# Kernel optimization log

Hardware: AMD Instinct MI355X
Metric: run time of the kernel (lower is better)

The kernel has to match this reference:

```python
import jax, jax.numpy as jnp
import numpy as np

D_HEAD = 64

def setup_inputs() -> dict:
    key = jax.random.key(0)
    kq, kk, kv, kc = jax.random.split(key, 4)
    B, H, T, D = 2, 16, 2048, D_HEAD
    Q = jax.random.normal(kq, (B, H, T, D), dtype=jnp.float32)
    K = jax.random.normal(kk, (B, H, T, D), dtype=jnp.float32)
    V = jax.random.normal(kv, (B, H, T, D), dtype=jnp.float32)
    # causal mask: True = attend
    mask = jnp.tril(jnp.ones((T, T), dtype=jnp.bool_))
    curvature = jax.random.normal(kc, (H, D, D), dtype=jnp.float32) * 0.02
    return {"Q": Q, "K": K, "V": V, "mask": mask, "curvature": curvature}

def reference(Q, K, V, mask, curvature):
    scale = 1.0 / np.sqrt(Q.shape[-1]).astype(np.float32)
    # per-head learned rotation of Q
    Q_rot = jnp.einsum('bhtd,hde->bhte', Q, curvature)
    scores = jnp.einsum('bhtd,bhsd->bhts', Q_rot, K) * scale  # [B,H,T,T]
    scores = jnp.where(mask[None, None, :, :], scores, -jnp.inf)
    attn = jax.nn.softmax(scores, axis=-1)
    out = jnp.einsum('bhts,bhsd->bhtd', attn, V)
    return out
```

## Files before the change

kernel.cpp:

```cpp
#include <hip/hip_runtime.h>


typedef __attribute__((ext_vector_type(8))) short short8;
typedef __attribute__((ext_vector_type(8))) unsigned short ushort8;
typedef __attribute__((ext_vector_type(4))) float f32x4;
typedef __attribute__((ext_vector_type(2))) _Float16 half2v;
typedef __attribute__((ext_vector_type(4))) _Float16 half4;
typedef __attribute__((ext_vector_type(8))) _Float16 half8;

constexpr int Tc = 2048;
constexpr int Dc = 64;
constexpr size_t REGION = (size_t)32 * Tc * Dc;

__device__ inline unsigned short f2bf(float f) {
    union { float f; unsigned u; } x; x.f = f;
    return (unsigned short)((x.u + 0x7fffu + ((x.u >> 16) & 1u)) >> 16);
}

__device__ inline half2v pkrtz(float a, float b) {
    return __builtin_bit_cast(half2v, __builtin_amdgcn_cvt_pkrtz(a, b));
}

#define MFMA_BF16_K32(a, b, c) __builtin_amdgcn_mfma_f32_16x16x32_bf16((a), (b), (c), 0, 0, 0)
#define MFMA_F16_K16(a, b, c)  __builtin_amdgcn_mfma_f32_16x16x16f16((a), (b), (c), 0, 0, 0)

__global__ __launch_bounds__(256, 1)
void holo_cfrag(const float* __restrict__ Cp, unsigned short* __restrict__ cfrag_g)
{
    const int t = threadIdx.x, lane = t & 63, eb = t >> 6;
    const int l15 = lane & 15, quad = lane >> 4;
    const int h = blockIdx.x;
    const float* Cg = Cp + (size_t)h * Dc * Dc;
    #pragma unroll
    for (int half = 0; half < 2; ++half) {
        short8 b;
        #pragma unroll
        for (int jj = 0; jj < 8; ++jj) {
            const int d = half * 32 + quad * 8 + jj;
            b[jj] = (short)f2bf(Cg[d * Dc + eb * 16 + l15]);
        }
        *(short8*)(&cfrag_g[(((size_t)h * 4 + eb) * 2 + half) * 512 + lane * 8]) = b;
    }
}

__global__ __launch_bounds__(256, 4)
void holo_prep8(const float* __restrict__ Qp, const float* __restrict__ Kp,
                const float* __restrict__ Vp,
                const unsigned short* __restrict__ cfrag_g,
                unsigned short* __restrict__ qfrag_g,
                unsigned short* __restrict__ kfrag_g,
                _Float16* __restrict__ vfrag_g)
{
    __shared__ unsigned short kt[64 * 72];
    __shared__ unsigned short qt[64 * 72];
    __shared__ _Float16      vt[64 * 72];
    __shared__ unsigned short pf[64 * 72];

    const int t = threadIdx.x, lane = t & 63, w = t >> 6;
    const int l15 = lane & 15, quad = lane >> 4, wb = w * 16;
    const int n = blockIdx.x, bh = n >> 5, st = n & 31, h = bh & 15;
    const int s0 = st * 64;

    const float* Qg = Qp + ((size_t)bh * Tc + s0) * Dc;
    const float* Kg = Kp + ((size_t)bh * Tc + s0) * Dc;
    const float* Vg = Vp + ((size_t)bh * Tc + s0) * Dc;

    #pragma unroll
    for (int kk = 0; kk < 4; ++kk) {
        const int flat = kk * 1024 + t * 4;
        const int r = flat >> 6, d0 = flat & 63;
        float4 kv = *(const float4*)(&Kg[flat]);
        ushort4 kp; kp.x = f2bf(kv.x); kp.y = f2bf(kv.y); kp.z = f2bf(kv.z); kp.w = f2bf(kv.w);
        *(ushort4*)(&kt[r * 72 + d0]) = kp;
        float4 qv = *(const float4*)(&Qg[flat]);
        ushort4 qp; qp.x = f2bf(qv.x); qp.y = f2bf(qv.y); qp.z = f2bf(qv.z); qp.w = f2bf(qv.w);
        *(ushort4*)(&qt[r * 72 + d0]) = qp;
        float4 vv = *(const float4*)(&Vg[flat]);
        half4 vp;
        vp[0] = (_Float16)vv.x; vp[1] = (_Float16)vv.y;
        vp[2] = (_Float16)vv.z; vp[3] = (_Float16)vv.w;
        *(half4*)(&vt[r * 72 + d0]) = vp;
    }
    __syncthreads();

    {
        const int row = wb + l15;
        ushort8 p0 = *(const ushort8*)(&kt[row * 72 + quad * 8]);
        ushort8 p1 = *(const ushort8*)(&kt[row * 72 + 32 + quad * 8]);
        unsigned short* kdst = kfrag_g + (((size_t)(bh * 32 + st) * 4 + w) * 64 + lane) * 16;
        *(ushort8*)(kdst) = p0;
        *(ushort8*)(kdst + 8) = p1;
    }

    {
        half8 v0, v1;
        #pragma unroll
        for (int dn = 0; dn < 2; ++dn)
            #pragma unroll
            for (int i = 0; i < 4; ++i)
                v0[dn * 4 + i] = vt[(wb + quad * 4 + i) * 72 + dn * 16 + l15];
        #pragma unroll
        for (int dn = 0; dn < 2; ++dn)
            #pragma unroll
            for (int i = 0; i < 4; ++i)
                v1[dn * 4 + i] = vt[(wb + quad * 4 + i) * 72 + (dn + 2) * 16 + l15];
        _Float16* vdst = vfrag_g + (((size_t)(bh * 32 + st) * 4 + w) * 64 + lane) * 16;
        *(half8*)(vdst) = v0;
        *(half8*)(vdst + 8) = v1;
    }

    {
        short8 a0 = *(const short8*)(&qt[(wb + l15) * 72 + quad * 8]);
        short8 a1 = *(const short8*)(&qt[(wb + l15) * 72 + 32 + quad * 8]);
        #pragma unroll
        for (int eb = 0; eb < 4; ++eb) {
            short8 b0 = *(const short8*)(&cfrag_g[(((size_t)h * 4 + eb) * 2 + 0) * 512 + lane * 8]);
            short8 b1 = *(const short8*)(&cfrag_g[(((size_t)h * 4 + eb) * 2 + 1) * 512 + lane * 8]);
            f32x4 c = {0.f, 0.f, 0.f, 0.f};
            c = MFMA_BF16_K32(a0, b0, c);
            c = MFMA_BF16_K32(a1, b1, c);
            #pragma unroll
            for (int i = 0; i < 4; ++i)
                pf[(wb + quad * 4 + i) * 72 + eb * 16 + l15] = f2bf(c[i] * 0.18033688f);
        }
        __threadfence_block();
        short8 fa0 = *(const short8*)(&pf[(wb + l15) * 72 + quad * 8]);
        short8 fa1 = *(const short8*)(&pf[(wb + l15) * 72 + 32 + quad * 8]);
        const size_t strip = (size_t)bh * 128 + st * 4 + w;
        *(short8*)(&qfrag_g[strip * 1024 + lane * 8]) = fa0;
        *(short8*)(&qfrag_g[strip * 1024 + 512 + lane * 8]) = fa1;
    }
}

__global__ __launch_bounds__(256, 4)
void holo_attn8(const unsigned short* __restrict__ qfrag_g,
                const unsigned short* __restrict__ kfrag_g,
                const _Float16* __restrict__ vfrag_g,
                float* __restrict__ Op)
{
    const int t = threadIdx.x, lane = t & 63, wid = t >> 6;
    const int l15 = lane & 15, quad = lane >> 4, wb = wid * 16;

    const int id = blockIdx.x;
    const int xcd = id & 7, m = (id >> 3) & 31, k = id >> 8;
    const int bh = xcd * 4 + k;
    const int mm = (k >= 2) ? ((m + 16) & 31) : m;
    const int qi = (k & 1) ? (31 - mm) : mm;
    const int q0 = qi * 64;

    short8 qa0, qa1;
    {
        const size_t strip = (size_t)bh * 128 + qi * 4 + wid;
        qa0 = *(const short8*)(&qfrag_g[strip * 1024 + lane * 8]);
        qa1 = *(const short8*)(&qfrag_g[strip * 1024 + 512 + lane * 8]);
    }

    const unsigned short* kbase = kfrag_g + (size_t)bh * 32 * 4 * 1024;
    const _Float16*       vbase = vfrag_g + (size_t)bh * 32 * 4 * 1024;

    f32x4 o[4];
    float l_lane = 0.f;
    #pragma unroll
    for (int dn = 0; dn < 4; ++dn) o[dn] = f32x4{0.f, 0.f, 0.f, 0.f};

    const int rowg = q0 + wb + l15;

    short8 kf0[4], kf1[4];
    half8 vlo[4], vhi[4];
    #pragma unroll
    for (int tn = 0; tn < 4; ++tn) {
        const unsigned short* kfb = kbase + ((size_t)tn * 64 + lane) * 16;
        kf0[tn] = *(const short8*)(kfb);
        kf1[tn] = *(const short8*)(kfb + 8);
        const _Float16* vfb = vbase + ((size_t)tn * 64 + lane) * 16;
        vlo[tn] = *(const half8*)(vfb);
        vhi[tn] = *(const half8*)(vfb + 8);
    }

    for (int j = 0; j <= qi; ++j) {
        f32x4 st[4];
        #pragma unroll
        for (int tn = 0; tn < 4; ++tn) {
            f32x4 c = {0.f, 0.f, 0.f, 0.f};
            c = MFMA_BF16_K32(kf0[tn], qa0, c);
            c = MFMA_BF16_K32(kf1[tn], qa1, c);
            st[tn] = c;
        }

        const int jn = (j < qi) ? j + 1 : j;
        #pragma unroll
        for (int tn = 0; tn < 4; ++tn) {
            const unsigned short* kfb = kbase + (size_t)jn * 4096 + ((size_t)tn * 64 + lane) * 16;
            kf0[tn] = *(const short8*)(kfb);
            kf1[tn] = *(const short8*)(kfb + 8);
        }

        half4 pa[4];
        #pragma unroll
        for (int tn = 0; tn < 4; ++tn) {
            float p[4];
            #pragma unroll
            for (int i = 0; i < 4; ++i) {
                float sv = st[tn][i];
                if (j == qi) {
                    const int colg = j * 64 + tn * 16 + quad * 4 + i;
                    if (colg > rowg) sv = -1e30f;
                }
                p[i] = __builtin_amdgcn_exp2f(sv);
                l_lane += p[i];
            }
            half2v lo = pkrtz(p[0], p[1]);
            half2v hi = pkrtz(p[2], p[3]);
            pa[tn] = __builtin_shufflevector(lo, hi, 0, 1, 2, 3);
        }

        #pragma unroll
        for (int tn = 0; tn < 4; ++tn) {
            half4 vf0 = __builtin_shufflevector(vlo[tn], vlo[tn], 0, 1, 2, 3);
            half4 vf1 = __builtin_shufflevector(vlo[tn], vlo[tn], 4, 5, 6, 7);
            half4 vf2 = __builtin_shufflevector(vhi[tn], vhi[tn], 0, 1, 2, 3);
            half4 vf3 = __builtin_shufflevector(vhi[tn], vhi[tn], 4, 5, 6, 7);
            o[0] = MFMA_F16_K16(vf0, pa[tn], o[0]);
            o[1] = MFMA_F16_K16(vf1, pa[tn], o[1]);
            o[2] = MFMA_F16_K16(vf2, pa[tn], o[2]);
            o[3] = MFMA_F16_K16(vf3, pa[tn], o[3]);
        }

        #pragma unroll
        for (int tn = 0; tn < 4; ++tn) {
            const _Float16* vfb = vbase + (size_t)jn * 4096 + ((size_t)tn * 64 + lane) * 16;
            vlo[tn] = *(const half8*)(vfb);
            vhi[tn] = *(const half8*)(vfb + 8);
        }
    }

    l_lane += __shfl_xor(l_lane, 16);
    l_lane += __shfl_xor(l_lane, 32);
    const float inv = 1.0f / l_lane;

    float* dst = Op + ((size_t)bh * Tc + rowg) * Dc;
    #pragma unroll
    for (int dn = 0; dn < 4; ++dn) {
        float4 r;
        r.x = o[dn][0] * inv; r.y = o[dn][1] * inv;
        r.z = o[dn][2] * inv; r.w = o[dn][3] * inv;
        *(float4*)(&dst[dn * 16 + quad * 4]) = r;
    }
}

extern "C" void kernel_launch(void* const* d_in, const int* in_sizes, int n_in,
                              void* d_out, int out_size, void* d_ws, size_t ws_size,
                              hipStream_t stream) {
    const float* Q = (const float*)d_in[0];
    const float* K = (const float*)d_in[1];
    const float* V = (const float*)d_in[2];
    const float* C = (const float*)d_in[4];
    float* O = (float*)d_out;

    unsigned short* qfrag_w = (unsigned short*)d_ws;
    unsigned short* kfrag_w = qfrag_w + REGION;
    _Float16*       vfrag_w = (_Float16*)(kfrag_w + REGION);
    unsigned short* cfrag_w = (unsigned short*)(vfrag_w + REGION);

    holo_cfrag<<<dim3(16), dim3(256), 0, stream>>>(C, cfrag_w);
    holo_prep8<<<dim3(1024), dim3(256), 0, stream>>>(Q, K, V, cfrag_w, qfrag_w, kfrag_w, vfrag_w);
    holo_attn8<<<dim3(1024), dim3(256), 0, stream>>>(qfrag_w, kfrag_w, vfrag_w, O);
}
```

Baseline: 145.7 us.

## Split causal key range into chunks with separate combine kernel

Each query tile's key loop is split into chunks of up to eight key tiles, launched as separate blocks (2560 total) that write unnormalized partial outputs and row sums to a workspace buffer. A new combine kernel sums the partials and normalizes. This targets load imbalance from the causal triangle, where late query tiles did all the work serially, and raises occupancy via launch bounds. It adds an extra launch and global-memory traffic for partials.

```diff
diff --git a/kernel.cpp b/kernel.cpp
--- a/kernel.cpp
+++ b/kernel.cpp
@@ -11,6 +11,7 @@
 constexpr int Tc = 2048;
 constexpr int Dc = 64;
 constexpr size_t REGION = (size_t)32 * Tc * Dc;
+constexpr int PSLOT = 4160;
 
 __device__ inline unsigned short f2bf(float f) {
     union { float f; unsigned u; } x; x.f = f;
@@ -132,20 +133,26 @@
     }
 }
 
-__global__ __launch_bounds__(256, 4)
-void holo_attn8(const unsigned short* __restrict__ qfrag_g,
-                const unsigned short* __restrict__ kfrag_g,
-                const _Float16* __restrict__ vfrag_g,
-                float* __restrict__ Op)
+__global__ __launch_bounds__(256, 8)
+void holo_attn10(const unsigned short* __restrict__ qfrag_g,
+                 const unsigned short* __restrict__ kfrag_g,
+                 const _Float16* __restrict__ vfrag_g,
+                 float* __restrict__ pbuf)
 {
     const int t = threadIdx.x, lane = t & 63, wid = t >> 6;
     const int l15 = lane & 15, quad = lane >> 4, wb = wid * 16;
 
     const int id = blockIdx.x;
-    const int xcd = id & 7, m = (id >> 3) & 31, k = id >> 8;
+    const int xcd = id & 7, r8 = id >> 3;
+    const int k = r8 & 3, c2 = r8 >> 2;
     const int bh = xcd * 4 + k;
-    const int mm = (k >= 2) ? ((m + 16) & 31) : m;
-    const int qi = (k & 1) ? (31 - mm) : mm;
+    int qi, c0;
+    if (c2 < 32)      { c0 = 0; qi = c2; }
+    else if (c2 < 56) { c0 = 1; qi = c2 - 24; }
+    else if (c2 < 72) { c0 = 2; qi = c2 - 40; }
+    else              { c0 = 3; qi = c2 - 48; }
+    const int j0 = c0 * 8;
+    const int jend = (j0 + 7 < qi) ? j0 + 7 : qi;
     const int q0 = qi * 64;
 
     short8 qa0, qa1;
@@ -169,15 +176,15 @@
     half8 vlo[4], vhi[4];
     #pragma unroll
     for (int tn = 0; tn < 4; ++tn) {
-        const unsigned short* kfb = kbase + ((size_t)tn * 64 + lane) * 16;
+        const unsigned short* kfb = kbase + (size_t)j0 * 4096 + ((size_t)tn * 64 + lane) * 16;
         kf0[tn] = *(const short8*)(kfb);
         kf1[tn] = *(const short8*)(kfb + 8);
-        const _Float16* vfb = vbase + ((size_t)tn * 64 + lane) * 16;
+        const _Float16* vfb = vbase + (size_t)j0 * 4096 + ((size_t)tn * 64 + lane) * 16;
         vlo[tn] = *(const half8*)(vfb);
         vhi[tn] = *(const half8*)(vfb + 8);
     }
 
-    for (int j = 0; j <= qi; ++j) {
+    for (int j = j0; j <= jend; ++j) {
         f32x4 st[4];
         #pragma unroll
         for (int tn = 0; tn < 4; ++tn) {
@@ -187,7 +194,7 @@
             st[tn] = c;
         }
 
-        const int jn = (j < qi) ? j + 1 : j;
+        const int jn = (j < jend) ? j + 1 : j;
         #pragma unroll
         for (int tn = 0; tn < 4; ++tn) {
             const unsigned short* kfb = kbase + (size_t)jn * 4096 + ((size_t)tn * 64 + lane) * 16;
@@ -234,18 +241,55 @@
         }
     }
 
+    float* ps = pbuf + ((size_t)bh * 80 + c2) * PSLOT;
+    #pragma unroll
+    for (int dn = 0; dn < 4; ++dn) {
+        float4 r;
+        r.x = o[dn][0]; r.y = o[dn][1]; r.z = o[dn][2]; r.w = o[dn][3];
+        *(float4*)(ps + (wb + l15) * 64 + dn * 16 + quad * 4) = r;
+    }
     l_lane += __shfl_xor(l_lane, 16);
     l_lane += __shfl_xor(l_lane, 32);
-    const float inv = 1.0f / l_lane;
-
-    float* dst = Op + ((size_t)bh * Tc + rowg) * Dc;
-    #pragma unroll
-    for (int dn = 0; dn < 4; ++dn) {
-        float4 r;
-        r.x = o[dn][0] * inv; r.y = o[dn][1] * inv;
-        r.z = o[dn][2] * inv; r.w = o[dn][3] * inv;
-        *(float4*)(&dst[dn * 16 + quad * 4]) = r;
-    }
+    if (quad == 0) ps[4096 + wb + l15] = l_lane;
+}
+
+__global__ __launch_bounds__(256, 8)
+void holo_comb(const float* __restrict__ pbuf, float* __restrict__ Op)
+{
+    const int id = blockIdx.x;
+    const int xcd = id & 7, rr = id >> 3;
+    const int bh = xcd * 4 + (rr & 3);
+    const int qi = rr >> 2;
+    const int t = threadIdx.x;
+    const int r = t >> 2, qq = t & 3;
+    const int nch = (qi >> 3) + 1;
+
+    float4 acc0 = {0,0,0,0}, acc1 = {0,0,0,0}, acc2 = {0,0,0,0}, acc3 = {0,0,0,0};
+    float lsum = 0.f;
+    for (int c = 0; c < nch; ++c) {
+        const int b4 = (c == 0) ? 0 : (c == 1) ? 24 : (c == 2) ? 40 : 48;
+        const float* ps = pbuf + ((size_t)bh * 80 + (b4 + qi)) * PSLOT;
+        lsum += ps[4096 + r];
+        const float* po = ps + r * 64 + qq * 16;
+        float4 a = *(const float4*)(po + 0);
+        float4 b = *(const float4*)(po + 4);
+        float4 cc = *(const float4*)(po + 8);
+        float4 d = *(const float4*)(po + 12);
+        acc0.x += a.x; acc0.y += a.y; acc0.z += a.z; acc0.w += a.w;
+        acc1.x += b.x; acc1.y += b.y; acc1.z += b.z; acc1.w += b.w;
+        acc2.x += cc.x; acc2.y += cc.y; acc2.z += cc.z; acc2.w += cc.w;
+        acc3.x += d.x; acc3.y += d.y; acc3.z += d.z; acc3.w += d.w;
+    }
+    const float inv = 1.0f / lsum;
+    float* dst = Op + ((size_t)bh * Tc + qi * 64 + r) * Dc + qq * 16;
+    acc0.x *= inv; acc0.y *= inv; acc0.z *= inv; acc0.w *= inv;
+    acc1.x *= inv; acc1.y *= inv; acc1.z *= inv; acc1.w *= inv;
+    acc2.x *= inv; acc2.y *= inv; acc2.z *= inv; acc2.w *= inv;
+    acc3.x *= inv; acc3.y *= inv; acc3.z *= inv; acc3.w *= inv;
+    *(float4*)(dst + 0)  = acc0;
+    *(float4*)(dst + 4)  = acc1;
+    *(float4*)(dst + 8)  = acc2;
+    *(float4*)(dst + 12) = acc3;
 }
 
 extern "C" void kernel_launch(void* const* d_in, const int* in_sizes, int n_in,
@@ -261,8 +305,10 @@
     unsigned short* kfrag_w = qfrag_w + REGION;
     _Float16*       vfrag_w = (_Float16*)(kfrag_w + REGION);
     unsigned short* cfrag_w = (unsigned short*)(vfrag_w + REGION);
+    float*          pbuf_w  = (float*)(cfrag_w + 16 * 4096);
 
     holo_cfrag<<<dim3(16), dim3(256), 0, stream>>>(C, cfrag_w);
     holo_prep8<<<dim3(1024), dim3(256), 0, stream>>>(Q, K, V, cfrag_w, qfrag_w, kfrag_w, vfrag_w);
-    holo_attn8<<<dim3(1024), dim3(256), 0, stream>>>(qfrag_w, kfrag_w, vfrag_w, O);
-}
+    holo_attn10<<<dim3(2560), dim3(256), 0, stream>>>(qfrag_w, kfrag_w, vfrag_w, pbuf_w);
+    holo_comb<<<dim3(1024), dim3(256), 0, stream>>>(pbuf_w, O);
+}
```

New measurement: 175.9 us. 20.7% more time.
